# Optimization experiments

Hardware: AMD Instinct MI355X
Metric: run time of the kernel (lower is better)

The kernel has to match this reference:

```python
import jax, jax.numpy as jnp
import numpy as np
from jax import lax

NUM_HEADS = 8
EPS_BN = 1e-5
EPS_LN = 1e-5


def setup_inputs() -> dict:
    key = jax.random.key(0)
    ks = iter(jax.random.split(key, 32))
    C = 512
    R = C // 16  # channel-gate reduction
    HID = 512    # classifier hidden
    NC = 1       # num_classes

    def gn(shape, scale=0.02):
        return (jax.random.normal(next(ks), shape, dtype=jnp.float32) * scale)

    inp = {
        "x": jax.random.normal(next(ks), (16, C, 28, 28), dtype=jnp.float32),
        # ChannelGate MLP (Linear(C,R) -> ReLU -> Linear(R,C))
        "mlp_w1": gn((R, C)), "mlp_b1": jnp.zeros((R,), jnp.float32),
        "mlp_w2": gn((C, R)), "mlp_b2": jnp.zeros((C,), jnp.float32),
        # SpatialGate 7x7 conv (2->1, no bias) + BatchNorm2d(1) eval-mode stats
        "sp_w": gn((1, 2, 7, 7)),
        "sp_gamma": jnp.ones((1,), jnp.float32), "sp_beta": jnp.zeros((1,), jnp.float32),
        "sp_mean": jnp.zeros((1,), jnp.float32), "sp_var": jnp.ones((1,), jnp.float32),
        # attention projections
        "wq": gn((C, C)), "bq": jnp.zeros((C,), jnp.float32),
        "wk": gn((C, C)), "bk": jnp.zeros((C,), jnp.float32),
        "wv": gn((C, C)), "bv": jnp.zeros((C,), jnp.float32),
        "wo": gn((C, C)), "bo": jnp.zeros((C,), jnp.float32),
        # classifier: LayerNorm(C) -> Linear(C,512) -> ReLU -> Linear(512,NC)
        "ln_g": jnp.ones((C,), jnp.float32), "ln_b": jnp.zeros((C,), jnp.float32),
        "fc1_w": gn((HID, C)), "fc1_b": jnp.zeros((HID,), jnp.float32),
        "fc2_w": gn((NC, HID)), "fc2_b": jnp.zeros((NC,), jnp.float32),
    }
    return inp


def reference(x, mlp_w1, mlp_b1, mlp_w2, mlp_b2, sp_w, sp_gamma, sp_beta,
              sp_mean, sp_var, wq, bq, wk, bk, wv, bv, wo, bo,
              ln_g, ln_b, fc1_w, fc1_b, fc2_w, fc2_b):
    B, C, H, W = x.shape
    N = H * W
    hd = C // NUM_HEADS

    # ---- CBAM: channel gate (avg + max global pools through shared MLP) ----
    def mlp(p):  # p: [B, C]
        return jax.nn.relu(p @ mlp_w1.T + mlp_b1) @ mlp_w2.T + mlp_b2

    avg_p = x.mean(axis=(2, 3))
    max_p = x.max(axis=(2, 3))
    ch_scale = jax.nn.sigmoid(mlp(avg_p) + mlp(max_p))[:, :, None, None]
    x = x * ch_scale

    # ---- CBAM: spatial gate ----
    comp = jnp.concatenate([x.max(axis=1, keepdims=True),
                            x.mean(axis=1, keepdims=True)], axis=1)  # [B,2,H,W]
    s = lax.conv_general_dilated(comp, sp_w, window_strides=(1, 1),
                                 padding=[(3, 3), (3, 3)],
                                 dimension_numbers=("NCHW", "OIHW", "NCHW"))
    s = (s - sp_mean[None, :, None, None]) * lax.rsqrt(sp_var + EPS_BN)[None, :, None, None]
    s = s * sp_gamma[None, :, None, None] + sp_beta[None, :, None, None]
    x = x * jax.nn.sigmoid(s)

    # ---- multi-head self-attention over HW tokens ----
    xf = x.reshape(B, C, N).transpose(0, 2, 1)  # [B, N, C]

    def heads(w, b):
        return (xf @ w.T + b).reshape(B, N, NUM_HEADS, hd).transpose(0, 2, 1, 3)

    Q, K, V = heads(wq, bq), heads(wk, bk), heads(wv, bv)  # [B, h, N, d]
    scores = jnp.einsum("bhnd,bhmd->bhnm", Q, K) / jnp.sqrt(jnp.float32(hd))
    attn = jax.nn.softmax(scores, axis=-1)  # dropout is identity in eval
    attended = jnp.einsum("bhnm,bhmd->bhnd", attn, V)
    attended = attended.transpose(0, 2, 1, 3).reshape(B, N, C)
    attended = attended @ wo.T + bo
    x = x + attended.transpose(0, 2, 1).reshape(B, C, H, W)

    # ---- classifier head ----
    p = x.mean(axis=(2, 3))  # AdaptiveAvgPool2d(1) + Flatten -> [B, C]
    mu = p.mean(axis=-1, keepdims=True)
    var = p.var(axis=-1, keepdims=True)
    ln = (p - mu) * lax.rsqrt(var + EPS_LN) * ln_g + ln_b
    h = jax.nn.relu(ln @ fc1_w.T + fc1_b)
    return h @ fc2_w.T + fc2_b
```

## Files before the change

kernel.cpp:

```cpp
#include <hip/hip_runtime.h>
#include <math.h>

#define BB 16
#define CC 512
#define HW 784
#define RR 32
#define NHD 8
#define HD 64
#define NT 784
#define NTILE 49
#define CBS 132

#define OFS_AVGP   0
#define OFS_MAXP   8192
#define OFS_CHS    16384
#define OFS_SP     49664
#define OFS_P1     62208
#define OFS_ABAR   70400
#define OFS_XG     78592
#define XG_SZ      (BB*CC*HW)
#define OFS_XGT    (OFS_XG + XG_SZ)
#define OFS_QBF    (OFS_XGT + XG_SZ/2)
#define OFS_KBF    (OFS_QBF + XG_SZ/2)
#define OFS_V2     (OFS_KBF + XG_SZ/2)
#define OFS_WF     (OFS_V2 + XG_SZ)
#define OFS_W      OFS_XG
#define OFS_PV     (OFS_XG + 131072)
#define OFS_CMAXP  (OFS_XG + 262144)
#define OFS_CMEANP (OFS_CMAXP + 200704)

typedef __attribute__((ext_vector_type(8))) short bf16x8;
typedef __attribute__((ext_vector_type(4))) float f32x4;

__device__ __forceinline__ unsigned short f2bf(float x) {
  union { float f; unsigned u; } v; v.f = x;
  unsigned r = v.u + 0x7fffu + ((v.u >> 16) & 1u);
  return (unsigned short)(r >> 16);
}
__device__ __forceinline__ float bf2f(unsigned short x) {
  union { unsigned u; float f; } v; v.u = ((unsigned)x) << 16;
  return v.f;
}
__device__ __forceinline__ void async16(const unsigned short* g, unsigned short* l) {
  __builtin_amdgcn_global_load_lds(
      (const __attribute__((address_space(1))) unsigned int*)g,
      (__attribute__((address_space(3))) unsigned int*)l, 16, 0, 0);
}

__global__ void k_pre(const float* __restrict__ x,
                      const float* __restrict__ wq, const float* __restrict__ wk,
                      const float* __restrict__ wv,
                      float* avg_p, float* max_p, unsigned short* __restrict__ Wf,
                      float* __restrict__ wsum, float* __restrict__ p1,
                      float* __restrict__ outp) {
  int bid = blockIdx.x;
  if (bid < 2048) {
    int wid = threadIdx.x >> 6;
    int lane = threadIdx.x & 63;
    int row = bid * 4 + wid;
    const float* xr = x + (size_t)row * HW;
    float s = 0.f, m = -INFINITY;
    for (int i = lane; i < HW; i += 64) { float v = xr[i]; s += v; m = fmaxf(m, v); }
    for (int o = 32; o; o >>= 1) { s += __shfl_down(s, o, 64); m = fmaxf(m, __shfl_down(m, o, 64)); }
    if (lane == 0) { avg_p[row] = s * (1.f/HW); max_p[row] = m; }
  } else if (bid < 2432) {
    int idx = (bid - 2048)*256 + threadIdx.x;
    int ln = idx & 63;
    int s  = (idx >> 6) & 15;
    int ct = (idx >> 10) & 31;
    int mat = idx >> 15;
    const float* W = (mat==0)? wq : (mat==1)? wk : wv;
    const float* src = W + (size_t)(ct*16 + (ln & 15))*CC + s*32 + (ln >> 4)*8;
    float4 f0 = *(const float4*)src;
    float4 f1 = *(const float4*)(src + 4);
    bf16x8 p;
    p[0]=(short)f2bf(f0.x); p[1]=(short)f2bf(f0.y); p[2]=(short)f2bf(f0.z); p[3]=(short)f2bf(f0.w);
    p[4]=(short)f2bf(f1.x); p[5]=(short)f2bf(f1.y); p[6]=(short)f2bf(f1.z); p[7]=(short)f2bf(f1.w);
    *(bf16x8*)(Wf + (size_t)idx*8) = p;
  } else {
    int idx = (bid - 2432)*256 + threadIdx.x;
    const float4 z = {0.f,0.f,0.f,0.f};
    if (idx < 4) *(float4*)&outp[idx*4] = z;
    for (int i = idx; i < 27136; i += 16384) {
      if (i < 25088) *(float4*)&wsum[(size_t)i*4] = z;
      else           *(float4*)&p1[(size_t)(i-25088)*4] = z;
    }
  }
}

__global__ void k_chmlp(const float* avg_p, const float* max_p,
                        const float* w1, const float* b1,
                        const float* w2, const float* b2, float* chs) {
  __shared__ float pa[CC], pm[CC], part[256], hr[64];
  int b = blockIdx.x, t = threadIdx.x;
  for (int i = t; i < CC; i += 256) { pa[i] = avg_p[b*CC+i]; pm[i] = max_p[b*CC+i]; }
  __syncthreads();
  {
    int rp = t & 63, ch = t >> 6;
    int r = rp & 31;
    const float* src = (rp < 32) ? pa : pm;
    const float* wr = w1 + (size_t)r*CC + ch*128;
    float s = 0.f;
    #pragma unroll 8
    for (int c = 0; c < 128; c++) s += src[ch*128 + c] * wr[c];
    part[t] = s;
  }
  __syncthreads();
  if (t < 64)
    hr[t] = fmaxf(part[t] + part[64+t] + part[128+t] + part[192+t] + b1[t & 31], 0.f);
  __syncthreads();
  for (int c = t; c < CC; c += 256) {
    float a = 2.f*b2[c];
    const float* wr = w2 + c*RR;
    #pragma unroll
    for (int r = 0; r < RR; r++) a += (hr[r]+hr[32+r])*wr[r];
    chs[b*CC+c] = 1.f/(1.f+__expf(-a));
  }
}

__global__ void k_chgatep(const float* __restrict__ x, const float* __restrict__ chs,
                          float* __restrict__ cmaxp, float* __restrict__ cmeanp) {
  __shared__ float cs[32];
  int b = blockIdx.x, cg = blockIdx.y, t = threadIdx.x;
  if (t < 32) cs[t] = chs[b*CC + cg*32 + t];
  __syncthreads();
  const float* xb = x + ((size_t)b*CC + cg*32)*HW;
  for (int pix = t; pix < HW; pix += 256) {
    float mx = -INFINITY, sm = 0.f;
    #pragma unroll
    for (int c = 0; c < 32; c++) {
      float v = xb[(size_t)c*HW + pix] * cs[c];
      mx = fmaxf(mx, v); sm += v;
    }
    cmaxp[(size_t)(cg*BB + b)*HW + pix] = mx;
    cmeanp[(size_t)(cg*BB + b)*HW + pix] = sm;
  }
}

__global__ void k_credsp(const float* __restrict__ cmaxp, const float* __restrict__ cmeanp,
                         const float* __restrict__ w, const float* g, const float* be,
                         const float* mu, const float* var, float* __restrict__ sp) {
  __shared__ float cmx[HW], cmn[HW];
  int b = blockIdx.x, q = blockIdx.y, t = threadIdx.x;
  for (int pix = t; pix < HW; pix += 256) {
    float mx = -INFINITY, sm = 0.f;
    #pragma unroll
    for (int cg = 0; cg < 16; cg++) {
      mx = fmaxf(mx, cmaxp[(size_t)(cg*BB + b)*HW + pix]);
      sm += cmeanp[(size_t)(cg*BB + b)*HW + pix];
    }
    cmx[pix] = mx; cmn[pix] = sm * (1.f/CC);
  }
  __syncthreads();
  if (t < 196) {
    int pix = q*196 + t;
    float bnscale = rsqrtf(var[0]+1e-5f)*g[0];
    int h = pix/28, wd = pix%28;
    float acc = 0.f;
    for (int kh = 0; kh < 7; kh++) {
      int ih = h + kh - 3; if (ih < 0 || ih >= 28) continue;
      for (int kw = 0; kw < 7; kw++) {
        int iw = wd + kw - 3; if (iw < 0 || iw >= 28) continue;
        int ip = ih*28+iw;
        acc += cmx[ip]*w[kh*7+kw] + cmn[ip]*w[49+kh*7+kw];
      }
    }
    float s = (acc - mu[0])*bnscale + be[0];
    sp[b*HW+pix] = 1.f/(1.f+__expf(-s));
  }
}

__global__ void k_sfuse(const float* __restrict__ x, const float* __restrict__ chs,
                        const float* __restrict__ sp, unsigned short* __restrict__ xgT,
                        float* __restrict__ p1) {
  __shared__ float cs[CC];
  int nt = blockIdx.x, b = blockIdx.y;
  int t = threadIdx.x, ln = t & 63;
  for (int i = t; i < CC; i += 256) cs[i] = chs[b*CC+i];
  __syncthreads();
  int n = nt*16 + (ln & 15);
  float spv = sp[b*HW + n];
  const float* xb = x + (size_t)b*CC*HW;
  #pragma unroll
  for (int i = 0; i < 4; i++) {
    int s = (t >> 6) + 4*i;
    int c = s*32 + (ln >> 4)*8;
    float vf[8];
    bf16x8 p;
    #pragma unroll
    for (int j = 0; j < 8; j++) {
      vf[j] = xb[(size_t)(c+j)*HW + n] * cs[c+j] * spv;
      p[j] = (short)f2bf(vf[j]);
    }
    *(bf16x8*)(xgT + ((((size_t)b*NTILE + nt)*16 + s)*64 + ln)*8) = p;
    #pragma unroll
    for (int j = 0; j < 8; j++) {
      float v = vf[j];
      v += __shfl_xor(v,1,64); v += __shfl_xor(v,2,64);
      v += __shfl_xor(v,4,64); v += __shfl_xor(v,8,64);
      vf[j] = v;
    }
    if ((ln & 15) == 0) {
      #pragma unroll
      for (int j = 0; j < 8; j++) atomicAdd(&p1[b*CC + c + j], vf[j]);
    }
  }
}

__global__ __launch_bounds__(256) void k_qkv_mfma(
    const unsigned short* __restrict__ xgT, const unsigned short* __restrict__ Wf,
    const float* __restrict__ bq, const float* __restrict__ bk, const float* __restrict__ bv,
    unsigned short* __restrict__ Qbf, unsigned short* __restrict__ Kbf,
    unsigned short* __restrict__ Vbf) {
  __shared__ __align__(16) unsigned char smem[65536];
  unsigned short* Alds = (unsigned short*)smem;
  float* Cb = (float*)smem;
  int blk = blockIdx.x;
  int yb = blk / 208;
  int r0 = blk % 208;
  int mt = r0 >> 4;
  int b  = r0 & 15;
  int mat = yb >> 1;
  int c0 = (yb & 1) * 256;
  int t = threadIdx.x, w = t >> 6, ln = t & 63;
  const unsigned short* Ab = xgT + (size_t)b*NTILE*8192;
  const unsigned short* Bb = Wf + (size_t)mat*32*8192;
  int ctgb = (c0 >> 4) + w*2;
  int ntc[4];
  #pragma unroll
  for (int m = 0; m < 4; m++) { int nt = 4*mt + m; ntc[m] = (nt > 48) ? 48 : nt; }
  #pragma unroll
  for (int j0 = 0; j0 < 16; j0++) {
    int j = w + 4*j0;
    int m = j >> 4, sj = j & 15;
    async16(Ab + (size_t)ntc[m]*8192 + (size_t)(sj*64 + ln)*8,
            Alds + (size_t)j*512);
  }
  f32x4 acc[4][4];
  #pragma unroll
  for (int m = 0; m < 4; m++)
    #pragma unroll
    for (int c2 = 0; c2 < 4; c2++) acc[m][c2] = (f32x4){0.f,0.f,0.f,0.f};
  __syncthreads();
  #pragma unroll 2
  for (int s = 0; s < 16; s++) {
    bf16x8 bf[4];
    bf[0] = *(const bf16x8*)(Bb + (size_t)((ctgb  )*16 + s)*512 + ln*8);
    bf[1] = *(const bf16x8*)(Bb + (size_t)((ctgb+1)*16 + s)*512 + ln*8);
    bf[2] = *(const bf16x8*)(Bb + (size_t)((ctgb+8)*16 + s)*512 + ln*8);
    bf[3] = *(const bf16x8*)(Bb + (size_t)((ctgb+9)*16 + s)*512 + ln*8);
    bf16x8 af[4];
    #pragma unroll
    for (int m = 0; m < 4; m++)
      af[m] = *(const bf16x8*)(Alds + (size_t)(m*16 + s)*512 + ln*8);
    #pragma unroll
    for (int m = 0; m < 4; m++) {
      #pragma unroll
      for (int c2 = 0; c2 < 4; c2++)
        acc[m][c2] = __builtin_amdgcn_mfma_f32_16x16x32_bf16(af[m], bf[c2], acc[m][c2], 0,0,0);
    }
  }
  __syncthreads();
  const float* bias = (mat==0)? bq : (mat==1)? bk : bv;
  #pragma unroll
  for (int ch = 0; ch < 2; ch++) {
    if (ch) __syncthreads();
    #pragma unroll
    for (int m = 0; m < 4; m++)
      #pragma unroll
      for (int c2 = 0; c2 < 2; c2++)
        #pragma unroll
        for (int r = 0; r < 4; r++)
          Cb[(m*16 + (ln>>4)*4 + r)*CBS + w*32 + c2*16 + (ln&15)] = acc[m][ch*2+c2][r];
    __syncthreads();
    #pragma unroll
    for (int i = 0; i < 4; i++) {
      int p = w*4 + i;
      int ntl = p >> 2, sl = p & 3;
      int nt = 4*mt + ntl;
      if (nt > 48) continue;
      int row = ntl*16 + (ln & 15);
      int col = sl*32 + (ln >> 4)*8;
      float4 v0 = *(const float4*)&Cb[row*CBS + col];
      float4 v1 = *(const float4*)&Cb[row*CBS + col + 4];
      float v[8] = {v0.x, v0.y, v0.z, v0.w, v1.x, v1.y, v1.z, v1.w};
      int colA = ch*128 + col;
      #pragma unroll
      for (int j = 0; j < 8; j++) v[j] += bias[c0 + colA + j];
      int token = nt*16 + (ln & 15);
      int h = (c0 >> 6) + (ch << 1) + (sl >> 1);
      int bh = b*NHD + h;
      bf16x8 pk;
      #pragma unroll
      for (int j = 0; j < 8; j++) pk[j] = (short)f2bf(v[j]);
      if (mat < 2) {
        unsigned short* Out = (mat == 0) ? Qbf : Kbf;
        *(bf16x8*)(Out + ((size_t)bh*NTILE + nt)*1024 + (size_t)(sl & 1)*512 + ln*8) = pk;
      } else {
        int d = (sl & 1)*32 + (ln >> 4)*8;
        *(bf16x8*)(Vbf + ((size_t)bh*NT + token)*HD + d) = pk;
      }
    }
  }
}

__global__ __launch_bounds__(256, 3) void k_attn8(const unsigned short* __restrict__ Qbf,
    const unsigned short* __restrict__ Kbf, float* __restrict__ wsum) {
  __shared__ float l_tmp[2][64];
  __shared__ float rl[2][16];
  int bh = blockIdx.x & 127, pg = blockIdx.x >> 7;
  int t = threadIdx.x, w = t >> 6, ln = t & 63;
  int ntA = pg*2;
  bool hasB = (ntA + 1) < NTILE;
  int ntB = hasB ? (ntA + 1) : ntA;
  const unsigned short* QbA = Qbf + ((size_t)bh*NTILE + ntA)*1024;
  const unsigned short* QbB = Qbf + ((size_t)bh*NTILE + ntB)*1024;
  const unsigned short* Kb = Kbf + (size_t)bh*NTILE*1024;
  bf16x8 qA0 = *(const bf16x8*)(QbA + ln*8);
  bf16x8 qA1 = *(const bf16x8*)(QbA + 512 + ln*8);
  bf16x8 qB0 = *(const bf16x8*)(QbB + ln*8);
  bf16x8 qB1 = *(const bf16x8*)(QbB + 512 + ln*8);
  f32x4 evA[13], evB[13];
  float lpA[4] = {0.f,0.f,0.f,0.f}, lpB[4] = {0.f,0.f,0.f,0.f};
  #pragma unroll
  for (int i = 0; i < 13; i++) {
    int mt = w + 4*i;
    bool valid = (i < 12) || (w == 0);
    int mtc = valid ? mt : 48;
    bf16x8 k0 = *(const bf16x8*)(Kb + (size_t)mtc*1024 + ln*8);
    bf16x8 k1 = *(const bf16x8*)(Kb + (size_t)mtc*1024 + 512 + ln*8);
    f32x4 a = {0.f,0.f,0.f,0.f};
    a = __builtin_amdgcn_mfma_f32_16x16x32_bf16(qA0, k0, a, 0,0,0);
    a = __builtin_amdgcn_mfma_f32_16x16x32_bf16(qA1, k1, a, 0,0,0);
    f32x4 c = {0.f,0.f,0.f,0.f};
    c = __builtin_amdgcn_mfma_f32_16x16x32_bf16(qB0, k0, c, 0,0,0);
    c = __builtin_amdgcn_mfma_f32_16x16x32_bf16(qB1, k1, c, 0,0,0);
    f32x4 ea, eb;
    #pragma unroll
    for (int r = 0; r < 4; r++) {
      ea[r] = __expf(a[r]*0.125f);
      eb[r] = __expf(c[r]*0.125f);
    }
    evA[i] = ea; evB[i] = eb;
    if (valid) {
      #pragma unroll
      for (int r = 0; r < 4; r++) { lpA[r] += ea[r]; lpB[r] += eb[r]; }
    }
  }
  #pragma unroll
  for (int r = 0; r < 4; r++) {
    float v = lpA[r];
    v += __shfl_xor(v,1,64); v += __shfl_xor(v,2,64);
    v += __shfl_xor(v,4,64); v += __shfl_xor(v,8,64);
    if ((ln & 15) == 0) l_tmp[0][w*16 + (ln>>4)*4 + r] = v;
    float u = lpB[r];
    u += __shfl_xor(u,1,64); u += __shfl_xor(u,2,64);
    u += __shfl_xor(u,4,64); u += __shfl_xor(u,8,64);
    if ((ln & 15) == 0) l_tmp[1][w*16 + (ln>>4)*4 + r] = u;
  }
  __syncthreads();
  if (t < 32) {
    int g = t >> 4, q = t & 15;
    rl[g][q] = 1.f / (l_tmp[g][q] + l_tmp[g][16+q] + l_tmp[g][32+q] + l_tmp[g][48+q]);
  }
  __syncthreads();
  f32x4 rlA = *(const f32x4*)&rl[0][(ln >> 4)*4];
  f32x4 rlB = *(const f32x4*)&rl[1][(ln >> 4)*4];
  #pragma unroll
  for (int i = 0; i < 13; i++) {
    int mt = w + 4*i;
    bool valid = (i < 12) || (w == 0);
    float v = evA[i][0]*rlA[0] + evA[i][1]*rlA[1] + evA[i][2]*rlA[2] + evA[i][3]*rlA[3];
    if (hasB)
      v += evB[i][0]*rlB[0] + evB[i][1]*rlB[1] + evB[i][2]*rlB[2] + evB[i][3]*rlB[3];
    v += __shfl_xor(v, 16, 64);
    v += __shfl_xor(v, 32, 64);
    if (valid && ln < 16)
      atomicAdd(&wsum[bh*NT + mt*16 + ln], v);
  }
}

__global__ void k_attn_av(const float* __restrict__ w, const unsigned short* __restrict__ Vm,
                          float* __restrict__ abar) {
  __shared__ float red[256];
  int bh = blockIdx.x, t = threadIdx.x;
  int d = t & 63, chunk = t >> 6;
  float acc = 0.f;
  const unsigned short* vb = Vm + (size_t)bh*NT*HD;
  const float* wb = w + bh*NT;
  for (int m = chunk*196; m < (chunk+1)*196; m++)
    acc += wb[m] * bf2f(vb[(size_t)m*HD + d]);
  red[t] = acc;
  __syncthreads();
  if (t < 64)
    abar[bh*HD + t] = (red[t] + red[64+t] + red[128+t] + red[192+t]) * (1.f/NT);
}

__global__ void k_headA(const float* __restrict__ p1, const float* __restrict__ abar,
                        const float* __restrict__ wo, const float* __restrict__ bo,
                        float* __restrict__ pv) {
  int b = blockIdx.x, cg = blockIdx.y;
  int t = threadIdx.x, w = t >> 6, ln = t & 63;
  float a[8];
  #pragma unroll
  for (int k = 0; k < 8; k++) a[k] = abar[b*CC + ln + 64*k];
  int c0 = cg*32 + w*8;
  for (int i = 0; i < 8; i++) {
    int c = c0 + i;
    const float* wr = wo + (size_t)c*CC;
    float s = 0.f;
    #pragma unroll
    for (int k = 0; k < 8; k++) s += a[k] * wr[ln + 64*k];
    for (int o = 32; o; o >>= 1) s += __shfl_down(s, o, 64);
    if (ln == 0) pv[b*CC + c] = s + bo[c] + p1[b*CC + c] * (1.f/HW);
  }
}

__global__ void k_headC(const float* __restrict__ pv, const float* __restrict__ ln_g,
                        const float* __restrict__ ln_b, const float* __restrict__ fc1_w,
                        const float* __restrict__ fc1_b, const float* __restrict__ fc2_w,
                        const float* __restrict__ fc2_b, float* __restrict__ out) {
  int b = blockIdx.x, cg = blockIdx.y;
  int t = threadIdx.x, w = t >> 6, ln = t & 63;
  float a[8];
  float s = 0.f, s2 = 0.f;
  #pragma unroll
  for (int k = 0; k < 8; k++) {
    a[k] = pv[b*CC + ln + 64*k];
    s += a[k]; s2 += a[k]*a[k];
  }
  for (int o = 32; o; o >>= 1) { s += __shfl_down(s, o, 64); s2 += __shfl_down(s2, o, 64); }
  s = __shfl(s, 0, 64); s2 = __shfl(s2, 0, 64);
  float mean = s * (1.f/CC);
  float rs = rsqrtf(s2*(1.f/CC) - mean*mean + 1e-5f);
  #pragma unroll
  for (int k = 0; k < 8; k++)
    a[k] = (a[k]-mean)*rs*ln_g[ln + 64*k] + ln_b[ln + 64*k];
  int c0 = cg*32 + w*8;
  float o2 = 0.f;
  for (int i = 0; i < 8; i++) {
    int c = c0 + i;
    const float* wr = fc1_w + (size_t)c*CC;
    float v = 0.f;
    #pragma unroll
    for (int k = 0; k < 8; k++) v += a[k] * wr[ln + 64*k];
    for (int o = 32; o; o >>= 1) v += __shfl_down(v, o, 64);
    if (ln == 0) o2 += fmaxf(v + fc1_b[c], 0.f) * fc2_w[c];
  }
  if (ln == 0) {
    if (cg == 0 && w == 0) o2 += fc2_b[0];
    atomicAdd(&out[b], o2);
  }
}

extern "C" void kernel_launch(void* const* d_in, const int* in_sizes, int n_in,
                              void* d_out, int out_size, void* d_ws, size_t ws_size,
                              hipStream_t stream) {
  const float* x       = (const float*)d_in[0];
  const float* mlp_w1  = (const float*)d_in[1];
  const float* mlp_b1  = (const float*)d_in[2];
  const float* mlp_w2  = (const float*)d_in[3];
  const float* mlp_b2  = (const float*)d_in[4];
  const float* sp_w    = (const float*)d_in[5];
  const float* sp_g    = (const float*)d_in[6];
  const float* sp_b    = (const float*)d_in[7];
  const float* sp_mu   = (const float*)d_in[8];
  const float* sp_var  = (const float*)d_in[9];
  const float* wq      = (const float*)d_in[10];
  const float* bq      = (const float*)d_in[11];
  const float* wk      = (const float*)d_in[12];
  const float* bk      = (const float*)d_in[13];
  const float* wv      = (const float*)d_in[14];
  const float* bv      = (const float*)d_in[15];
  const float* wo      = (const float*)d_in[16];
  const float* bo      = (const float*)d_in[17];
  const float* ln_g    = (const float*)d_in[18];
  const float* ln_b    = (const float*)d_in[19];
  const float* fc1_w   = (const float*)d_in[20];
  const float* fc1_b   = (const float*)d_in[21];
  const float* fc2_w   = (const float*)d_in[22];
  const float* fc2_b   = (const float*)d_in[23];

  float* ws = (float*)d_ws;
  float* avg_p = ws + OFS_AVGP;
  float* max_p = ws + OFS_MAXP;
  float* chs   = ws + OFS_CHS;
  float* sp    = ws + OFS_SP;
  float* p1    = ws + OFS_P1;
  float* abar  = ws + OFS_ABAR;
  unsigned short* xgT = (unsigned short*)(ws + OFS_XGT);
  unsigned short* Qbf = (unsigned short*)(ws + OFS_QBF);
  unsigned short* Kbf = (unsigned short*)(ws + OFS_KBF);
  unsigned short* Vbf = (unsigned short*)(ws + OFS_V2);
  unsigned short* Wf  = (unsigned short*)(ws + OFS_WF);
  float* wsum  = ws + OFS_W;
  float* pv    = ws + OFS_PV;
  float* cmaxp = ws + OFS_CMAXP;
  float* cmeanp= ws + OFS_CMEANP;

  k_pre    <<<2496, 256, 0, stream>>>(x, wq, wk, wv, avg_p, max_p, Wf, wsum, p1,
                                      (float*)d_out);
  k_chmlp  <<<BB, 256, 0, stream>>>(avg_p, max_p, mlp_w1, mlp_b1, mlp_w2, mlp_b2, chs);
  k_chgatep<<<dim3(BB,16), 256, 0, stream>>>(x, chs, cmaxp, cmeanp);
  k_credsp <<<dim3(BB,4), 256, 0, stream>>>(cmaxp, cmeanp, sp_w, sp_g, sp_b, sp_mu, sp_var, sp);
  k_sfuse  <<<dim3(NTILE,BB), 256, 0, stream>>>(x, chs, sp, xgT, p1);
  k_qkv_mfma<<<1248, 256, 0, stream>>>(xgT, Wf, bq, bk, bv, Qbf, Kbf, Vbf);
  k_attn8  <<<25*128, 256, 0, stream>>>(Qbf, Kbf, wsum);
  k_attn_av<<<128, 256, 0, stream>>>(wsum, Vbf, abar);
  k_headA  <<<dim3(BB,16), 256, 0, stream>>>(p1, abar, wo, bo, pv);
  k_headC  <<<dim3(BB,16), 256, 0, stream>>>(pv, ln_g, ln_b, fc1_w, fc1_b,
                                             fc2_w, fc2_b, (float*)d_out);
}
```

Baseline: 276.9 us.

## Fuse all stages into one cooperative persistent kernel with grid syncs

Replaces the ten separate kernel launches with a single cooperative persistent kernel. The kernel strides over each stage's work items and separates stages with grid-wide syncs, removing per-launch overhead and inter-kernel gaps. The grid is capped at up to 2 blocks per CU times 256, which leaves far fewer blocks for large stages like the attention and QKV GEMM, so it can lose latency hiding. It also uses 64KB of static shared memory, which may cut occupancy. The original multi-kernel path is kept as a fallback if the cooperative launch fails.

```diff
diff --git a/kernel.cpp b/kernel.cpp
--- a/kernel.cpp
+++ b/kernel.cpp
@@ -1,4 +1,5 @@
 #include <hip/hip_runtime.h>
+#include <hip/hip_cooperative_groups.h>
 #include <math.h>
 
 #define BB 16
@@ -45,6 +46,425 @@
   __builtin_amdgcn_global_load_lds(
       (const __attribute__((address_space(1))) unsigned int*)g,
       (__attribute__((address_space(3))) unsigned int*)l, 16, 0, 0);
+}
+
+struct MegaArgs {
+  const float *x, *mlp_w1, *mlp_b1, *mlp_w2, *mlp_b2;
+  const float *sp_w, *sp_g, *sp_bb, *sp_mu, *sp_var;
+  const float *wq, *bq, *wk, *bk, *wv, *bv, *wo, *bo;
+  const float *ln_g, *ln_b, *fc1_w, *fc1_b, *fc2_w, *fc2_b;
+  float *avg_p, *max_p, *chs, *sp, *p1, *abar, *wsum, *pv, *out;
+  float *cmaxp, *cmeanp;
+  unsigned short *xgT, *Qbf, *Kbf, *Vbf, *Wf;
+};
+
+__global__ __launch_bounds__(256) void k_mega(MegaArgs A) {
+  __shared__ __align__(16) unsigned char smem[65536];
+  cooperative_groups::grid_group gg = cooperative_groups::this_grid();
+  const int bid = blockIdx.x, gdim = gridDim.x;
+  const int t = threadIdx.x, w = t >> 6, ln = t & 63;
+
+  for (int wk = bid; wk < 2048; wk += gdim) {
+    int row = wk*4 + w;
+    const float* xr = A.x + (size_t)row * HW;
+    float s = 0.f, m = -INFINITY;
+    for (int i = ln; i < HW; i += 64) { float v = xr[i]; s += v; m = fmaxf(m, v); }
+    for (int o = 32; o; o >>= 1) { s += __shfl_down(s, o, 64); m = fmaxf(m, __shfl_down(m, o, 64)); }
+    if (ln == 0) { A.avg_p[row] = s * (1.f/HW); A.max_p[row] = m; }
+  }
+  for (int wk = bid; wk < 384; wk += gdim) {
+    int idx = wk*256 + t;
+    int l2 = idx & 63;
+    int s  = (idx >> 6) & 15;
+    int ct = (idx >> 10) & 31;
+    int mat = idx >> 15;
+    const float* W = (mat==0)? A.wq : (mat==1)? A.wk : A.wv;
+    const float* src = W + (size_t)(ct*16 + (l2 & 15))*CC + s*32 + (l2 >> 4)*8;
+    float4 f0 = *(const float4*)src;
+    float4 f1 = *(const float4*)(src + 4);
+    bf16x8 p;
+    p[0]=(short)f2bf(f0.x); p[1]=(short)f2bf(f0.y); p[2]=(short)f2bf(f0.z); p[3]=(short)f2bf(f0.w);
+    p[4]=(short)f2bf(f1.x); p[5]=(short)f2bf(f1.y); p[6]=(short)f2bf(f1.z); p[7]=(short)f2bf(f1.w);
+    *(bf16x8*)(A.Wf + (size_t)idx*8) = p;
+  }
+  {
+    const float4 z = {0.f,0.f,0.f,0.f};
+    for (int i = bid*256 + t; i < 27136; i += gdim*256) {
+      if (i < 25088) *(float4*)&A.wsum[(size_t)i*4] = z;
+      else           *(float4*)&A.p1[(size_t)(i-25088)*4] = z;
+    }
+    if (bid == 0 && t < BB) A.out[t] = 0.f;
+  }
+  gg.sync();
+
+  {
+    float* pa = (float*)smem; float* pm = pa + CC; float* part = pm + CC; float* hr = part + 256;
+    for (int wk = bid; wk < 16; wk += gdim) {
+      int b = wk;
+      for (int i = t; i < CC; i += 256) { pa[i] = A.avg_p[b*CC+i]; pm[i] = A.max_p[b*CC+i]; }
+      __syncthreads();
+      {
+        int rp = t & 63, ch = t >> 6;
+        int r = rp & 31;
+        const float* src = (rp < 32) ? pa : pm;
+        const float* wr = A.mlp_w1 + (size_t)r*CC + ch*128;
+        float s = 0.f;
+        #pragma unroll 8
+        for (int c = 0; c < 128; c++) s += src[ch*128 + c] * wr[c];
+        part[t] = s;
+      }
+      __syncthreads();
+      if (t < 64)
+        hr[t] = fmaxf(part[t] + part[64+t] + part[128+t] + part[192+t] + A.mlp_b1[t & 31], 0.f);
+      __syncthreads();
+      for (int c = t; c < CC; c += 256) {
+        float a = 2.f*A.mlp_b2[c];
+        const float* wr = A.mlp_w2 + c*RR;
+        #pragma unroll
+        for (int r = 0; r < RR; r++) a += (hr[r]+hr[32+r])*wr[r];
+        A.chs[b*CC+c] = 1.f/(1.f+__expf(-a));
+      }
+      __syncthreads();
+    }
+  }
+  gg.sync();
+
+  {
+    float* cs = (float*)smem;
+    for (int wk = bid; wk < 512; wk += gdim) {
+      int pr = wk >> 1, half = wk & 1;
+      int b = pr & 15, cg = pr >> 4;
+      if (t < 32) cs[t] = A.chs[b*CC + cg*32 + t];
+      __syncthreads();
+      const float* xb = A.x + ((size_t)b*CC + cg*32)*HW;
+      for (int pix = half*392 + t; pix < half*392 + 392; pix += 256) {
+        float mx = -INFINITY, sm = 0.f;
+        #pragma unroll
+        for (int c = 0; c < 32; c++) {
+          float v = xb[(size_t)c*HW + pix] * cs[c];
+          mx = fmaxf(mx, v); sm += v;
+        }
+        A.cmaxp[(size_t)(cg*BB + b)*HW + pix] = mx;
+        A.cmeanp[(size_t)(cg*BB + b)*HW + pix] = sm;
+      }
+      __syncthreads();
+    }
+  }
+  gg.sync();
+
+  {
+    float* cmx = (float*)smem; float* cmn = cmx + HW;
+    for (int wk = bid; wk < 64; wk += gdim) {
+      int b = wk & 15, q = wk >> 4;
+      for (int pix = t; pix < HW; pix += 256) {
+        float mx = -INFINITY, sm = 0.f;
+        #pragma unroll
+        for (int cg = 0; cg < 16; cg++) {
+          mx = fmaxf(mx, A.cmaxp[(size_t)(cg*BB + b)*HW + pix]);
+          sm += A.cmeanp[(size_t)(cg*BB + b)*HW + pix];
+        }
+        cmx[pix] = mx; cmn[pix] = sm * (1.f/CC);
+      }
+      __syncthreads();
+      if (t < 196) {
+        int pix = q*196 + t;
+        float bnscale = rsqrtf(A.sp_var[0]+1e-5f)*A.sp_g[0];
+        int h = pix/28, wd = pix%28;
+        float acc = 0.f;
+        for (int kh = 0; kh < 7; kh++) {
+          int ih = h + kh - 3; if (ih < 0 || ih >= 28) continue;
+          for (int kw = 0; kw < 7; kw++) {
+            int iw = wd + kw - 3; if (iw < 0 || iw >= 28) continue;
+            int ip = ih*28+iw;
+            acc += cmx[ip]*A.sp_w[kh*7+kw] + cmn[ip]*A.sp_w[49+kh*7+kw];
+          }
+        }
+        float s = (acc - A.sp_mu[0])*bnscale + A.sp_bb[0];
+        A.sp[b*HW+pix] = 1.f/(1.f+__expf(-s));
+      }
+      __syncthreads();
+    }
+  }
+  gg.sync();
+
+  {
+    float* cs = (float*)smem;
+    for (int wk = bid; wk < 784; wk += gdim) {
+      int nt = wk % 49, b = wk / 49;
+      for (int i = t; i < CC; i += 256) cs[i] = A.chs[b*CC+i];
+      __syncthreads();
+      int n = nt*16 + (ln & 15);
+      float spv = A.sp[b*HW + n];
+      const float* xb = A.x + (size_t)b*CC*HW;
+      #pragma unroll
+      for (int i = 0; i < 4; i++) {
+        int s = (t >> 6) + 4*i;
+        int c = s*32 + (ln >> 4)*8;
+        float vf[8];
+        bf16x8 p;
+        #pragma unroll
+        for (int j = 0; j < 8; j++) {
+          vf[j] = xb[(size_t)(c+j)*HW + n] * cs[c+j] * spv;
+          p[j] = (short)f2bf(vf[j]);
+        }
+        *(bf16x8*)(A.xgT + ((((size_t)b*NTILE + nt)*16 + s)*64 + ln)*8) = p;
+        #pragma unroll
+        for (int j = 0; j < 8; j++) {
+          float v = vf[j];
+          v += __shfl_xor(v,1,64); v += __shfl_xor(v,2,64);
+          v += __shfl_xor(v,4,64); v += __shfl_xor(v,8,64);
+          vf[j] = v;
+        }
+        if ((ln & 15) == 0) {
+          #pragma unroll
+          for (int j = 0; j < 8; j++) atomicAdd(&A.p1[b*CC + c + j], vf[j]);
+        }
+      }
+      __syncthreads();
+    }
+  }
+  gg.sync();
+
+  {
+    unsigned short* Alds = (unsigned short*)smem;
+    float* Cb = (float*)smem;
+    for (int blk = bid; blk < 1248; blk += gdim) {
+      __syncthreads();
+      int yb = blk / 208;
+      int r0 = blk % 208;
+      int mt = r0 >> 4;
+      int b  = r0 & 15;
+      int mat = yb >> 1;
+      int c0 = (yb & 1) * 256;
+      const unsigned short* Ab = A.xgT + (size_t)b*NTILE*8192;
+      const unsigned short* Bb = A.Wf + (size_t)mat*32*8192;
+      int ctgb = (c0 >> 4) + w*2;
+      int ntc[4];
+      #pragma unroll
+      for (int m = 0; m < 4; m++) { int nt = 4*mt + m; ntc[m] = (nt > 48) ? 48 : nt; }
+      #pragma unroll
+      for (int j0 = 0; j0 < 16; j0++) {
+        int j = w + 4*j0;
+        int m = j >> 4, sj = j & 15;
+        async16(Ab + (size_t)ntc[m]*8192 + (size_t)(sj*64 + ln)*8,
+                Alds + (size_t)j*512);
+      }
+      f32x4 acc[4][4];
+      #pragma unroll
+      for (int m = 0; m < 4; m++)
+        #pragma unroll
+        for (int c2 = 0; c2 < 4; c2++) acc[m][c2] = (f32x4){0.f,0.f,0.f,0.f};
+      __syncthreads();
+      #pragma unroll 2
+      for (int s = 0; s < 16; s++) {
+        bf16x8 bf[4];
+        bf[0] = *(const bf16x8*)(Bb + (size_t)((ctgb  )*16 + s)*512 + ln*8);
+        bf[1] = *(const bf16x8*)(Bb + (size_t)((ctgb+1)*16 + s)*512 + ln*8);
+        bf[2] = *(const bf16x8*)(Bb + (size_t)((ctgb+8)*16 + s)*512 + ln*8);
+        bf[3] = *(const bf16x8*)(Bb + (size_t)((ctgb+9)*16 + s)*512 + ln*8);
+        bf16x8 af[4];
+        #pragma unroll
+        for (int m = 0; m < 4; m++)
+          af[m] = *(const bf16x8*)(Alds + (size_t)(m*16 + s)*512 + ln*8);
+        #pragma unroll
+        for (int m = 0; m < 4; m++) {
+          #pragma unroll
+          for (int c2 = 0; c2 < 4; c2++)
+            acc[m][c2] = __builtin_amdgcn_mfma_f32_16x16x32_bf16(af[m], bf[c2], acc[m][c2], 0,0,0);
+        }
+      }
+      __syncthreads();
+      const float* bias = (mat==0)? A.bq : (mat==1)? A.bk : A.bv;
+      #pragma unroll
+      for (int ch = 0; ch < 2; ch++) {
+        if (ch) __syncthreads();
+        #pragma unroll
+        for (int m = 0; m < 4; m++)
+          #pragma unroll
+          for (int c2 = 0; c2 < 2; c2++)
+            #pragma unroll
+            for (int r = 0; r < 4; r++)
+              Cb[(m*16 + (ln>>4)*4 + r)*CBS + w*32 + c2*16 + (ln&15)] = acc[m][ch*2+c2][r];
+        __syncthreads();
+        #pragma unroll
+        for (int i = 0; i < 4; i++) {
+          int p = w*4 + i;
+          int ntl = p >> 2, sl = p & 3;
+          int nt = 4*mt + ntl;
+          if (nt > 48) continue;
+          int row = ntl*16 + (ln & 15);
+          int col = sl*32 + (ln >> 4)*8;
+          float4 v0 = *(const float4*)&Cb[row*CBS + col];
+          float4 v1 = *(const float4*)&Cb[row*CBS + col + 4];
+          float v[8] = {v0.x, v0.y, v0.z, v0.w, v1.x, v1.y, v1.z, v1.w};
+          int colA = ch*128 + col;
+          #pragma unroll
+          for (int j = 0; j < 8; j++) v[j] += bias[c0 + colA + j];
+          int token = nt*16 + (ln & 15);
+          int h = (c0 >> 6) + (ch << 1) + (sl >> 1);
+          int bh = b*NHD + h;
+          bf16x8 pk;
+          #pragma unroll
+          for (int j = 0; j < 8; j++) pk[j] = (short)f2bf(v[j]);
+          if (mat < 2) {
+            unsigned short* Out = (mat == 0) ? A.Qbf : A.Kbf;
+            *(bf16x8*)(Out + ((size_t)bh*NTILE + nt)*1024 + (size_t)(sl & 1)*512 + ln*8) = pk;
+          } else {
+            int d = (sl & 1)*32 + (ln >> 4)*8;
+            *(bf16x8*)(A.Vbf + ((size_t)bh*NT + token)*HD + d) = pk;
+          }
+        }
+      }
+    }
+  }
+  gg.sync();
+
+  {
+    float* lt  = (float*)smem;
+    float* rlp = lt + 128;
+    for (int wk = bid; wk < 3200; wk += gdim) {
+      int bh = wk & 127, pg = wk >> 7;
+      int ntA = pg*2;
+      bool hasB = (ntA + 1) < NTILE;
+      int ntB = hasB ? (ntA + 1) : ntA;
+      const unsigned short* QbA = A.Qbf + ((size_t)bh*NTILE + ntA)*1024;
+      const unsigned short* QbB = A.Qbf + ((size_t)bh*NTILE + ntB)*1024;
+      const unsigned short* Kb = A.Kbf + (size_t)bh*NTILE*1024;
+      bf16x8 qA0 = *(const bf16x8*)(QbA + ln*8);
+      bf16x8 qA1 = *(const bf16x8*)(QbA + 512 + ln*8);
+      bf16x8 qB0 = *(const bf16x8*)(QbB + ln*8);
+      bf16x8 qB1 = *(const bf16x8*)(QbB + 512 + ln*8);
+      f32x4 evA[13], evB[13];
+      float lpA[4] = {0.f,0.f,0.f,0.f}, lpB[4] = {0.f,0.f,0.f,0.f};
+      #pragma unroll
+      for (int i = 0; i < 13; i++) {
+        int mt = w + 4*i;
+        bool valid = (i < 12) || (w == 0);
+        int mtc = valid ? mt : 48;
+        bf16x8 k0 = *(const bf16x8*)(Kb + (size_t)mtc*1024 + ln*8);
+        bf16x8 k1 = *(const bf16x8*)(Kb + (size_t)mtc*1024 + 512 + ln*8);
+        f32x4 a = {0.f,0.f,0.f,0.f};
+        a = __builtin_amdgcn_mfma_f32_16x16x32_bf16(qA0, k0, a, 0,0,0);
+        a = __builtin_amdgcn_mfma_f32_16x16x32_bf16(qA1, k1, a, 0,0,0);
+        f32x4 c = {0.f,0.f,0.f,0.f};
+        c = __builtin_amdgcn_mfma_f32_16x16x32_bf16(qB0, k0, c, 0,0,0);
+        c = __builtin_amdgcn_mfma_f32_16x16x32_bf16(qB1, k1, c, 0,0,0);
+        f32x4 ea, eb;
+        #pragma unroll
+        for (int r = 0; r < 4; r++) {
+          ea[r] = __expf(a[r]*0.125f);
+          eb[r] = __expf(c[r]*0.125f);
+        }
+        evA[i] = ea; evB[i] = eb;
+        if (valid) {
+          #pragma unroll
+          for (int r = 0; r < 4; r++) { lpA[r] += ea[r]; lpB[r] += eb[r]; }
+        }
+      }
+      #pragma unroll
+      for (int r = 0; r < 4; r++) {
+        float v = lpA[r];
+        v += __shfl_xor(v,1,64); v += __shfl_xor(v,2,64);
+        v += __shfl_xor(v,4,64); v += __shfl_xor(v,8,64);
+        if ((ln & 15) == 0) lt[w*16 + (ln>>4)*4 + r] = v;
+        float u = lpB[r];
+        u += __shfl_xor(u,1,64); u += __shfl_xor(u,2,64);
+        u += __shfl_xor(u,4,64); u += __shfl_xor(u,8,64);
+        if ((ln & 15) == 0) lt[64 + w*16 + (ln>>4)*4 + r] = u;
+      }
+      __syncthreads();
+      if (t < 32) {
+        int g = t >> 4, q = t & 15;
+        rlp[g*16 + q] = 1.f / (lt[g*64+q] + lt[g*64+16+q] + lt[g*64+32+q] + lt[g*64+48+q]);
+      }
+      __syncthreads();
+      f32x4 rlA = *(const f32x4*)&rlp[(ln >> 4)*4];
+      f32x4 rlB = *(const f32x4*)&rlp[16 + (ln >> 4)*4];
+      #pragma unroll
+      for (int i = 0; i < 13; i++) {
+        int mt = w + 4*i;
+        bool valid = (i < 12) || (w == 0);
+        float v = evA[i][0]*rlA[0] + evA[i][1]*rlA[1] + evA[i][2]*rlA[2] + evA[i][3]*rlA[3];
+        if (hasB)
+          v += evB[i][0]*rlB[0] + evB[i][1]*rlB[1] + evB[i][2]*rlB[2] + evB[i][3]*rlB[3];
+        v += __shfl_xor(v, 16, 64);
+        v += __shfl_xor(v, 32, 64);
+        if (valid && ln < 16)
+          atomicAdd(&A.wsum[bh*NT + mt*16 + ln], v);
+      }
+    }
+  }
+  gg.sync();
+
+  {
+    float* red = (float*)smem;
+    for (int wk = bid; wk < 128; wk += gdim) {
+      int bh = wk;
+      int d = t & 63, chunk = t >> 6;
+      float acc = 0.f;
+      const unsigned short* vb = A.Vbf + (size_t)bh*NT*HD;
+      const float* wb = A.wsum + bh*NT;
+      for (int m = chunk*196; m < (chunk+1)*196; m++)
+        acc += wb[m] * bf2f(vb[(size_t)m*HD + d]);
+      red[t] = acc;
+      __syncthreads();
+      if (t < 64)
+        A.abar[bh*HD + t] = (red[t] + red[64+t] + red[128+t] + red[192+t]) * (1.f/NT);
+      __syncthreads();
+    }
+  }
+  gg.sync();
+
+  for (int wk = bid; wk < 256; wk += gdim) {
+    int b = wk & 15, cg = wk >> 4;
+    float a[8];
+    #pragma unroll
+    for (int k = 0; k < 8; k++) a[k] = A.abar[b*CC + ln + 64*k];
+    int c0 = cg*32 + w*8;
+    for (int i = 0; i < 8; i++) {
+      int c = c0 + i;
+      const float* wr = A.wo + (size_t)c*CC;
+      float s = 0.f;
+      #pragma unroll
+      for (int k = 0; k < 8; k++) s += a[k] * wr[ln + 64*k];
+      for (int o = 32; o; o >>= 1) s += __shfl_down(s, o, 64);
+      if (ln == 0) A.pv[b*CC + c] = s + A.bo[c] + A.p1[b*CC + c] * (1.f/HW);
+    }
+  }
+  gg.sync();
+
+  for (int wk = bid; wk < 256; wk += gdim) {
+    int b = wk & 15, cg = wk >> 4;
+    float a[8];
+    float s = 0.f, s2 = 0.f;
+    #pragma unroll
+    for (int k = 0; k < 8; k++) {
+      a[k] = A.pv[b*CC + ln + 64*k];
+      s += a[k]; s2 += a[k]*a[k];
+    }
+    for (int o = 32; o; o >>= 1) { s += __shfl_down(s, o, 64); s2 += __shfl_down(s2, o, 64); }
+    s = __shfl(s, 0, 64); s2 = __shfl(s2, 0, 64);
+    float mean = s * (1.f/CC);
+    float rs = rsqrtf(s2*(1.f/CC) - mean*mean + 1e-5f);
+    #pragma unroll
+    for (int k = 0; k < 8; k++)
+      a[k] = (a[k]-mean)*rs*A.ln_g[ln + 64*k] + A.ln_b[ln + 64*k];
+    int c0 = cg*32 + w*8;
+    float o2 = 0.f;
+    for (int i = 0; i < 8; i++) {
+      int c = c0 + i;
+      const float* wr = A.fc1_w + (size_t)c*CC;
+      float v = 0.f;
+      #pragma unroll
+      for (int k = 0; k < 8; k++) v += a[k] * wr[ln + 64*k];
+      for (int o = 32; o; o >>= 1) v += __shfl_down(v, o, 64);
+      if (ln == 0) o2 += fmaxf(v + A.fc1_b[c], 0.f) * A.fc2_w[c];
+    }
+    if (ln == 0) {
+      if (cg == 0 && w == 0) o2 += A.fc2_b[0];
+      atomicAdd(&A.out[b], o2);
+    }
+  }
 }
 
 __global__ void k_pre(const float* __restrict__ x,
@@ -498,16 +918,44 @@
   float* cmaxp = ws + OFS_CMAXP;
   float* cmeanp= ws + OFS_CMEANP;
 
-  k_pre    <<<2496, 256, 0, stream>>>(x, wq, wk, wv, avg_p, max_p, Wf, wsum, p1,
-                                      (float*)d_out);
-  k_chmlp  <<<BB, 256, 0, stream>>>(avg_p, max_p, mlp_w1, mlp_b1, mlp_w2, mlp_b2, chs);
-  k_chgatep<<<dim3(BB,16), 256, 0, stream>>>(x, chs, cmaxp, cmeanp);
-  k_credsp <<<dim3(BB,4), 256, 0, stream>>>(cmaxp, cmeanp, sp_w, sp_g, sp_b, sp_mu, sp_var, sp);
-  k_sfuse  <<<dim3(NTILE,BB), 256, 0, stream>>>(x, chs, sp, xgT, p1);
-  k_qkv_mfma<<<1248, 256, 0, stream>>>(xgT, Wf, bq, bk, bv, Qbf, Kbf, Vbf);
-  k_attn8  <<<25*128, 256, 0, stream>>>(Qbf, Kbf, wsum);
-  k_attn_av<<<128, 256, 0, stream>>>(wsum, Vbf, abar);
-  k_headA  <<<dim3(BB,16), 256, 0, stream>>>(p1, abar, wo, bo, pv);
-  k_headC  <<<dim3(BB,16), 256, 0, stream>>>(pv, ln_g, ln_b, fc1_w, fc1_b,
-                                             fc2_w, fc2_b, (float*)d_out);
-}
+  static int coopGrid = -2;
+  if (coopGrid == -2) {
+    int nb = 0;
+    if (hipOccupancyMaxActiveBlocksPerMultiprocessor(&nb, k_mega, 256, 0) != hipSuccess)
+      nb = 0;
+    coopGrid = (nb >= 1) ? (nb > 2 ? 2 : nb) * 256 : -1;
+  }
+
+  bool ok = false;
+  if (coopGrid > 0) {
+    MegaArgs A;
+    A.x = x; A.mlp_w1 = mlp_w1; A.mlp_b1 = mlp_b1; A.mlp_w2 = mlp_w2; A.mlp_b2 = mlp_b2;
+    A.sp_w = sp_w; A.sp_g = sp_g; A.sp_bb = sp_b; A.sp_mu = sp_mu; A.sp_var = sp_var;
+    A.wq = wq; A.bq = bq; A.wk = wk; A.bk = bk; A.wv = wv; A.bv = bv; A.wo = wo; A.bo = bo;
+    A.ln_g = ln_g; A.ln_b = ln_b; A.fc1_w = fc1_w; A.fc1_b = fc1_b; A.fc2_w = fc2_w; A.fc2_b = fc2_b;
+    A.avg_p = avg_p; A.max_p = max_p; A.chs = chs; A.sp = sp; A.p1 = p1; A.abar = abar;
+    A.wsum = wsum; A.pv = pv; A.out = (float*)d_out;
+    A.cmaxp = cmaxp; A.cmeanp = cmeanp;
+    A.xgT = xgT; A.Qbf = Qbf; A.Kbf = Kbf; A.Vbf = Vbf; A.Wf = Wf;
+    void* kargs[] = { (void*)&A };
+    hipError_t e = hipLaunchCooperativeKernel((const void*)k_mega, dim3(coopGrid),
+                                              dim3(256), kargs, 0, stream);
+    ok = (e == hipSuccess);
+    if (!ok) coopGrid = -1;
+  }
+
+  if (!ok) {
+    k_pre    <<<2496, 256, 0, stream>>>(x, wq, wk, wv, avg_p, max_p, Wf, wsum, p1,
+                                        (float*)d_out);
+    k_chmlp  <<<BB, 256, 0, stream>>>(avg_p, max_p, mlp_w1, mlp_b1, mlp_w2, mlp_b2, chs);
+    k_chgatep<<<dim3(BB,16), 256, 0, stream>>>(x, chs, cmaxp, cmeanp);
+    k_credsp <<<dim3(BB,4), 256, 0, stream>>>(cmaxp, cmeanp, sp_w, sp_g, sp_b, sp_mu, sp_var, sp);
+    k_sfuse  <<<dim3(NTILE,BB), 256, 0, stream>>>(x, chs, sp, xgT, p1);
+    k_qkv_mfma<<<1248, 256, 0, stream>>>(xgT, Wf, bq, bk, bv, Qbf, Kbf, Vbf);
+    k_attn8  <<<25*128, 256, 0, stream>>>(Qbf, Kbf, wsum);
+    k_attn_av<<<128, 256, 0, stream>>>(wsum, Vbf, abar);
+    k_headA  <<<dim3(BB,16), 256, 0, stream>>>(p1, abar, wo, bo, pv);
+    k_headC  <<<dim3(BB,16), 256, 0, stream>>>(pv, ln_g, ln_b, fc1_w, fc1_b,
+                                               fc2_w, fc2_b, (float*)d_out);
+  }
+}
```

Result: no change. 280.1 us (+1.1%).

## Fuse channel MLP, gate pooling and spatial conv into fewer kernels; widen QKV blocks

Applied to the files above, without the earlier changes.

Replaces four small kernels (channel MLP, channel-gated pooling, spatial conv reduction, scaling fuse) with two. Each block recomputes the tiny channel MLP redundantly, and the spatial 7x7 conv is computed locally per 16-token tile from only the needed rows. This removes two launches and the chs/sp round trips through global memory. Separately, the QKV MFMA kernel moves to 512 threads per block, with each wave holding half as many accumulators, to raise occupancy. The cost is redundant MLP work and repeated partial-row reductions across 784 blocks.

```diff
diff --git a/kernel.cpp b/kernel.cpp
--- a/kernel.cpp
+++ b/kernel.cpp
@@ -13,8 +13,6 @@
 
 #define OFS_AVGP   0
 #define OFS_MAXP   8192
-#define OFS_CHS    16384
-#define OFS_SP     49664
 #define OFS_P1     62208
 #define OFS_ABAR   70400
 #define OFS_XG     78592
@@ -88,11 +86,13 @@
   }
 }
 
-__global__ void k_chmlp(const float* avg_p, const float* max_p,
-                        const float* w1, const float* b1,
-                        const float* w2, const float* b2, float* chs) {
-  __shared__ float pa[CC], pm[CC], part[256], hr[64];
-  int b = blockIdx.x, t = threadIdx.x;
+__global__ void k_chgate2(const float* __restrict__ x,
+                          const float* __restrict__ avg_p, const float* __restrict__ max_p,
+                          const float* __restrict__ w1, const float* __restrict__ b1,
+                          const float* __restrict__ w2, const float* __restrict__ b2,
+                          float* __restrict__ cmaxp, float* __restrict__ cmeanp) {
+  __shared__ float pa[CC], pm[CC], part[256], hr[64], cs[32];
+  int b = blockIdx.x, cg = blockIdx.y, t = threadIdx.x;
   for (int i = t; i < CC; i += 256) { pa[i] = avg_p[b*CC+i]; pm[i] = max_p[b*CC+i]; }
   __syncthreads();
   {
@@ -109,51 +109,81 @@
   if (t < 64)
     hr[t] = fmaxf(part[t] + part[64+t] + part[128+t] + part[192+t] + b1[t & 31], 0.f);
   __syncthreads();
+  if (t < 32) {
+    int c = cg*32 + t;
+    float a = 2.f*b2[c];
+    const float* wr = w2 + c*RR;
+    #pragma unroll
+    for (int r = 0; r < RR; r++) a += (hr[r]+hr[32+r])*wr[r];
+    cs[t] = 1.f/(1.f+__expf(-a));
+  }
+  __syncthreads();
+  const float* xb = x + ((size_t)b*CC + cg*32)*HW;
+  for (int pix = t; pix < HW; pix += 256) {
+    float mx = -INFINITY, sm = 0.f;
+    #pragma unroll
+    for (int c = 0; c < 32; c++) {
+      float v = xb[(size_t)c*HW + pix] * cs[c];
+      mx = fmaxf(mx, v); sm += v;
+    }
+    cmaxp[(size_t)(cg*BB + b)*HW + pix] = mx;
+    cmeanp[(size_t)(cg*BB + b)*HW + pix] = sm;
+  }
+}
+
+__global__ void k_sfusesp(const float* __restrict__ x,
+                          const float* __restrict__ avg_p, const float* __restrict__ max_p,
+                          const float* __restrict__ w1, const float* __restrict__ b1,
+                          const float* __restrict__ w2, const float* __restrict__ b2,
+                          const float* __restrict__ cmaxp, const float* __restrict__ cmeanp,
+                          const float* __restrict__ wsp, const float* g, const float* be,
+                          const float* mu, const float* var,
+                          unsigned short* __restrict__ xgT, float* __restrict__ p1) {
+  __shared__ float pa[CC], pm[CC], part[256], hr[64], cs[CC];
+  __shared__ float cmx[224], cmn[224], spl[16];
+  int nt = blockIdx.x, b = blockIdx.y;
+  int t = threadIdx.x, ln = t & 63;
+  for (int i = t; i < CC; i += 256) { pa[i] = avg_p[b*CC+i]; pm[i] = max_p[b*CC+i]; }
+  __syncthreads();
+  {
+    int rp = t & 63, ch = t >> 6;
+    int r = rp & 31;
+    const float* src = (rp < 32) ? pa : pm;
+    const float* wr = w1 + (size_t)r*CC + ch*128;
+    float s = 0.f;
+    #pragma unroll 8
+    for (int c = 0; c < 128; c++) s += src[ch*128 + c] * wr[c];
+    part[t] = s;
+  }
+  __syncthreads();
+  if (t < 64)
+    hr[t] = fmaxf(part[t] + part[64+t] + part[128+t] + part[192+t] + b1[t & 31], 0.f);
+  __syncthreads();
   for (int c = t; c < CC; c += 256) {
     float a = 2.f*b2[c];
     const float* wr = w2 + c*RR;
     #pragma unroll
     for (int r = 0; r < RR; r++) a += (hr[r]+hr[32+r])*wr[r];
-    chs[b*CC+c] = 1.f/(1.f+__expf(-a));
-  }
-}
-
-__global__ void k_chgatep(const float* __restrict__ x, const float* __restrict__ chs,
-                          float* __restrict__ cmaxp, float* __restrict__ cmeanp) {
-  __shared__ float cs[32];
-  int b = blockIdx.x, cg = blockIdx.y, t = threadIdx.x;
-  if (t < 32) cs[t] = chs[b*CC + cg*32 + t];
-  __syncthreads();
-  const float* xb = x + ((size_t)b*CC + cg*32)*HW;
-  for (int pix = t; pix < HW; pix += 256) {
-    float mx = -INFINITY, sm = 0.f;
-    #pragma unroll
-    for (int c = 0; c < 32; c++) {
-      float v = xb[(size_t)c*HW + pix] * cs[c];
-      mx = fmaxf(mx, v); sm += v;
-    }
-    cmaxp[(size_t)(cg*BB + b)*HW + pix] = mx;
-    cmeanp[(size_t)(cg*BB + b)*HW + pix] = sm;
-  }
-}
-
-__global__ void k_credsp(const float* __restrict__ cmaxp, const float* __restrict__ cmeanp,
-                         const float* __restrict__ w, const float* g, const float* be,
-                         const float* mu, const float* var, float* __restrict__ sp) {
-  __shared__ float cmx[HW], cmn[HW];
-  int b = blockIdx.x, q = blockIdx.y, t = threadIdx.x;
-  for (int pix = t; pix < HW; pix += 256) {
+    cs[c] = 1.f/(1.f+__expf(-a));
+  }
+  int n0 = nt*16, n1 = nt*16 + 15;
+  int h0 = n0/28, h1 = n1/28;
+  int rlo = (h0 >= 3) ? h0-3 : 0;
+  int rhi = (h1+3 <= 27) ? h1+3 : 27;
+  int npix = (rhi - rlo + 1) * 28;
+  for (int idx = t; idx < npix; idx += 256) {
+    int pix = rlo*28 + idx;
     float mx = -INFINITY, sm = 0.f;
     #pragma unroll
     for (int cg = 0; cg < 16; cg++) {
       mx = fmaxf(mx, cmaxp[(size_t)(cg*BB + b)*HW + pix]);
       sm += cmeanp[(size_t)(cg*BB + b)*HW + pix];
     }
-    cmx[pix] = mx; cmn[pix] = sm * (1.f/CC);
-  }
-  __syncthreads();
-  if (t < 196) {
-    int pix = q*196 + t;
+    cmx[idx] = mx; cmn[idx] = sm * (1.f/CC);
+  }
+  __syncthreads();
+  if (t < 16) {
+    int pix = nt*16 + t;
     float bnscale = rsqrtf(var[0]+1e-5f)*g[0];
     int h = pix/28, wd = pix%28;
     float acc = 0.f;
@@ -161,25 +191,16 @@
       int ih = h + kh - 3; if (ih < 0 || ih >= 28) continue;
       for (int kw = 0; kw < 7; kw++) {
         int iw = wd + kw - 3; if (iw < 0 || iw >= 28) continue;
-        int ip = ih*28+iw;
-        acc += cmx[ip]*w[kh*7+kw] + cmn[ip]*w[49+kh*7+kw];
+        int lidx = (ih - rlo)*28 + iw;
+        acc += cmx[lidx]*wsp[kh*7+kw] + cmn[lidx]*wsp[49+kh*7+kw];
       }
     }
     float s = (acc - mu[0])*bnscale + be[0];
-    sp[b*HW+pix] = 1.f/(1.f+__expf(-s));
-  }
-}
-
-__global__ void k_sfuse(const float* __restrict__ x, const float* __restrict__ chs,
-                        const float* __restrict__ sp, unsigned short* __restrict__ xgT,
-                        float* __restrict__ p1) {
-  __shared__ float cs[CC];
-  int nt = blockIdx.x, b = blockIdx.y;
-  int t = threadIdx.x, ln = t & 63;
-  for (int i = t; i < CC; i += 256) cs[i] = chs[b*CC+i];
+    spl[t] = 1.f/(1.f+__expf(-s));
+  }
   __syncthreads();
   int n = nt*16 + (ln & 15);
-  float spv = sp[b*HW + n];
+  float spv = spl[ln & 15];
   const float* xb = x + (size_t)b*CC*HW;
   #pragma unroll
   for (int i = 0; i < 4; i++) {
@@ -207,7 +228,7 @@
   }
 }
 
-__global__ __launch_bounds__(256) void k_qkv_mfma(
+__global__ __launch_bounds__(512) void k_qkv_mfma(
     const unsigned short* __restrict__ xgT, const unsigned short* __restrict__ Wf,
     const float* __restrict__ bq, const float* __restrict__ bk, const float* __restrict__ bv,
     unsigned short* __restrict__ Qbf, unsigned short* __restrict__ Kbf,
@@ -222,42 +243,39 @@
   int b  = r0 & 15;
   int mat = yb >> 1;
   int c0 = (yb & 1) * 256;
-  int t = threadIdx.x, w = t >> 6, ln = t & 63;
+  int t = threadIdx.x, w8 = t >> 6, ln = t & 63;
+  int g = w8 >> 2, wq = w8 & 3;
   const unsigned short* Ab = xgT + (size_t)b*NTILE*8192;
   const unsigned short* Bb = Wf + (size_t)mat*32*8192;
-  int ctgb = (c0 >> 4) + w*2;
+  int cb = (c0 >> 4) + g*8 + wq*2;
   int ntc[4];
   #pragma unroll
   for (int m = 0; m < 4; m++) { int nt = 4*mt + m; ntc[m] = (nt > 48) ? 48 : nt; }
   #pragma unroll
-  for (int j0 = 0; j0 < 16; j0++) {
-    int j = w + 4*j0;
+  for (int j0 = 0; j0 < 8; j0++) {
+    int j = w8 + 8*j0;
     int m = j >> 4, sj = j & 15;
     async16(Ab + (size_t)ntc[m]*8192 + (size_t)(sj*64 + ln)*8,
             Alds + (size_t)j*512);
   }
-  f32x4 acc[4][4];
+  f32x4 acc[4][2];
   #pragma unroll
   for (int m = 0; m < 4; m++)
     #pragma unroll
-    for (int c2 = 0; c2 < 4; c2++) acc[m][c2] = (f32x4){0.f,0.f,0.f,0.f};
+    for (int c2 = 0; c2 < 2; c2++) acc[m][c2] = (f32x4){0.f,0.f,0.f,0.f};
   __syncthreads();
   #pragma unroll 2
   for (int s = 0; s < 16; s++) {
-    bf16x8 bf[4];
-    bf[0] = *(const bf16x8*)(Bb + (size_t)((ctgb  )*16 + s)*512 + ln*8);
-    bf[1] = *(const bf16x8*)(Bb + (size_t)((ctgb+1)*16 + s)*512 + ln*8);
-    bf[2] = *(const bf16x8*)(Bb + (size_t)((ctgb+8)*16 + s)*512 + ln*8);
-    bf[3] = *(const bf16x8*)(Bb + (size_t)((ctgb+9)*16 + s)*512 + ln*8);
+    bf16x8 bf0 = *(const bf16x8*)(Bb + (size_t)((cb  )*16 + s)*512 + ln*8);
+    bf16x8 bf1 = *(const bf16x8*)(Bb + (size_t)((cb+1)*16 + s)*512 + ln*8);
     bf16x8 af[4];
     #pragma unroll
     for (int m = 0; m < 4; m++)
       af[m] = *(const bf16x8*)(Alds + (size_t)(m*16 + s)*512 + ln*8);
     #pragma unroll
     for (int m = 0; m < 4; m++) {
-      #pragma unroll
-      for (int c2 = 0; c2 < 4; c2++)
-        acc[m][c2] = __builtin_amdgcn_mfma_f32_16x16x32_bf16(af[m], bf[c2], acc[m][c2], 0,0,0);
+      acc[m][0] = __builtin_amdgcn_mfma_f32_16x16x32_bf16(af[m], bf0, acc[m][0], 0,0,0);
+      acc[m][1] = __builtin_amdgcn_mfma_f32_16x16x32_bf16(af[m], bf1, acc[m][1], 0,0,0);
     }
   }
   __syncthreads();
@@ -265,17 +283,19 @@
   #pragma unroll
   for (int ch = 0; ch < 2; ch++) {
     if (ch) __syncthreads();
-    #pragma unroll
-    for (int m = 0; m < 4; m++)
+    if (g == ch) {
       #pragma unroll
-      for (int c2 = 0; c2 < 2; c2++)
+      for (int m = 0; m < 4; m++)
         #pragma unroll
-        for (int r = 0; r < 4; r++)
-          Cb[(m*16 + (ln>>4)*4 + r)*CBS + w*32 + c2*16 + (ln&15)] = acc[m][ch*2+c2][r];
+        for (int c2 = 0; c2 < 2; c2++)
+          #pragma unroll
+          for (int r = 0; r < 4; r++)
+            Cb[(m*16 + (ln>>4)*4 + r)*CBS + wq*32 + c2*16 + (ln&15)] = acc[m][c2][r];
+    }
     __syncthreads();
     #pragma unroll
-    for (int i = 0; i < 4; i++) {
-      int p = w*4 + i;
+    for (int i = 0; i < 2; i++) {
+      int p = w8*2 + i;
       int ntl = p >> 2, sl = p & 3;
       int nt = 4*mt + ntl;
       if (nt > 48) continue;
@@ -484,8 +504,6 @@
   float* ws = (float*)d_ws;
   float* avg_p = ws + OFS_AVGP;
   float* max_p = ws + OFS_MAXP;
-  float* chs   = ws + OFS_CHS;
-  float* sp    = ws + OFS_SP;
   float* p1    = ws + OFS_P1;
   float* abar  = ws + OFS_ABAR;
   unsigned short* xgT = (unsigned short*)(ws + OFS_XGT);
@@ -500,11 +518,13 @@
 
   k_pre    <<<2496, 256, 0, stream>>>(x, wq, wk, wv, avg_p, max_p, Wf, wsum, p1,
                                       (float*)d_out);
-  k_chmlp  <<<BB, 256, 0, stream>>>(avg_p, max_p, mlp_w1, mlp_b1, mlp_w2, mlp_b2, chs);
-  k_chgatep<<<dim3(BB,16), 256, 0, stream>>>(x, chs, cmaxp, cmeanp);
-  k_credsp <<<dim3(BB,4), 256, 0, stream>>>(cmaxp, cmeanp, sp_w, sp_g, sp_b, sp_mu, sp_var, sp);
-  k_sfuse  <<<dim3(NTILE,BB), 256, 0, stream>>>(x, chs, sp, xgT, p1);
-  k_qkv_mfma<<<1248, 256, 0, stream>>>(xgT, Wf, bq, bk, bv, Qbf, Kbf, Vbf);
+  k_chgate2<<<dim3(BB,16), 256, 0, stream>>>(x, avg_p, max_p, mlp_w1, mlp_b1,
+                                             mlp_w2, mlp_b2, cmaxp, cmeanp);
+  k_sfusesp<<<dim3(NTILE,BB), 256, 0, stream>>>(x, avg_p, max_p, mlp_w1, mlp_b1,
+                                                mlp_w2, mlp_b2, cmaxp, cmeanp,
+                                                sp_w, sp_g, sp_b, sp_mu, sp_var,
+                                                xgT, p1);
+  k_qkv_mfma<<<1248, 512, 0, stream>>>(xgT, Wf, bq, bk, bv, Qbf, Kbf, Vbf);
   k_attn8  <<<25*128, 256, 0, stream>>>(Qbf, Kbf, wsum);
   k_attn_av<<<128, 256, 0, stream>>>(wsum, Vbf, abar);
   k_headA  <<<dim3(BB,16), 256, 0, stream>>>(p1, abar, wo, bo, pv);
```

Measured after the change: 287.5 us. 1.04x slower.
